# Kernel tuning notes

Hardware: AMD Instinct MI355X
Metric: run time of the kernel (lower is better)

The kernel has to match this reference:

```python
import jax, jax.numpy as jnp
import numpy as np

B, CIN, COUT, H, W, K, G = 2, 256, 256, 128, 128, 3, 4
PAD = (K - 1) // 2


def setup_inputs() -> dict:
    key = jax.random.key(0)
    k1, k2, k3, k4 = jax.random.split(key, 4)
    x = jax.random.normal(k1, (B, CIN, H, W), dtype=jnp.float32)
    # conv_offset: 1x1 conv, out channels = G*2*K*K. (Zero-init in the module; use
    # small random weights so offsets are non-trivial for correctness testing.)
    w_offset = jax.random.normal(k2, (G * 2 * K * K, CIN), dtype=jnp.float32) * 0.01
    b_offset = jax.random.normal(k3, (G * 2 * K * K,), dtype=jnp.float32) * 0.5
    # DeformConv weight (bias=False in mmcv DeformConv)
    w_deform = jax.random.normal(k4, (COUT, CIN, K, K), dtype=jnp.float32) * (1.0 / np.sqrt(CIN * K * K))
    return {"x": x, "w_offset": w_offset, "b_offset": b_offset, "w_deform": w_deform}


def _bilinear_gather(img, y, x):
    """img: [B,G,Cg,H,W]; y,x: [B,G,H,W] float sample coords -> [B,G,Cg,H,W].
    Zero padding outside the image (mmcv DCN bilinear semantics)."""
    b, g, cg, h, w = img.shape
    imgf = img.reshape(b, g, cg, h * w)
    y0 = jnp.floor(y)
    x0 = jnp.floor(x)
    out = jnp.zeros((b, g, cg, h * w), img.dtype)
    for yy, xx in ((y0, x0), (y0, x0 + 1.0), (y0 + 1.0, x0), (y0 + 1.0, x0 + 1.0)):
        wgt = (1.0 - jnp.abs(y - yy)) * (1.0 - jnp.abs(x - xx))
        valid = (yy >= 0) & (yy < h) & (xx >= 0) & (xx < w)
        wgt = jnp.where(valid, wgt, 0.0)
        yi = jnp.clip(yy, 0, h - 1).astype(jnp.int32)
        xi = jnp.clip(xx, 0, w - 1).astype(jnp.int32)
        idx = (yi * w + xi).reshape(b, g, 1, h * w)
        vals = jnp.take_along_axis(imgf, jnp.broadcast_to(idx, (b, g, cg, h * w)), axis=3)
        out = out + wgt.reshape(b, g, 1, h * w) * vals
    return out.reshape(b, g, cg, h, w)


def reference(x, w_offset, b_offset, w_deform):
    b, cin, h, w = x.shape
    cout, _, k, _ = w_deform.shape
    pad = (k - 1) // 2
    # 1x1 offset conv
    offset = jnp.einsum('bchw,oc->bohw', x, w_offset) + b_offset[None, :, None, None]
    g = offset.shape[1] // (2 * k * k)
    off = offset.reshape(b, g, k * k, 2, h, w)  # (dy, dx) per kernel tap, mmcv layout
    xg = x.reshape(b, g, cin // g, h, w)
    hh = jnp.arange(h, dtype=x.dtype)[:, None]
    ww = jnp.arange(w, dtype=x.dtype)[None, :]
    out = jnp.zeros((b, cout, h, w), x.dtype)
    for i in range(k):
        for j in range(k):
            t = i * k + j
            ys = hh - pad + i + off[:, :, t, 0]  # [B,G,H,W]
            xs = ww - pad + j + off[:, :, t, 1]
            samp = _bilinear_gather(xg, ys, xs).reshape(b, cin, h, w)
            out = out + jnp.einsum('bchw,oc->bohw', samp, w_deform[:, :, i, j])
    return jax.nn.relu(out)
```

## Files before the change

kernel.cpp:

```cpp
#include <hip/hip_runtime.h>
#include <stdint.h>

#define HW    16384
#define CIN   256
#define COUT  256
#define Hh    128
#define Ww    128
#define OFFC  72

typedef __attribute__((ext_vector_type(4))) float    f32x4;
typedef __attribute__((ext_vector_type(2))) _Float16 f16x2;
typedef __attribute__((ext_vector_type(8))) _Float16 f16x8;
typedef unsigned short u16;
typedef unsigned int   u32;

__device__ __forceinline__ u16 f2h(float f) { return __builtin_bit_cast(u16, (_Float16)f); }
__device__ __forceinline__ u32 pk2(float f) { u32 h = f2h(f); return h | (h << 16); }
__device__ __forceinline__ f16x2 bch(u32 u) { return __builtin_bit_cast(f16x2, u); }

__global__ __launch_bounds__(256) void kprep(const float* __restrict__ x, const float* __restrict__ wd,
                                             const float* __restrict__ wo, u16* __restrict__ xt,
                                             u16* __restrict__ wfrag, u16* __restrict__ wfrag2) {
  __shared__ float smem[9216];
  int blk = blockIdx.x;
  if (blk < 2048) {
    int bg = blk >> 8;
    int p0 = (blk & 255) << 6;
    const float* src = x + (size_t)bg * 64 * HW + p0;
    #pragma unroll
    for (int r = 0; r < 16; ++r) {
      int idx = threadIdx.x + 256 * r;
      int c = idx >> 6, px = idx & 63;
      smem[c * 65 + px] = src[(size_t)c * HW + px];
    }
    __syncthreads();
    int px = threadIdx.x >> 2, seg = threadIdx.x & 3;
    u32 w[8];
    #pragma unroll
    for (int k = 0; k < 8; ++k) {
      float lo = smem[(seg * 16 + 2 * k) * 65 + px];
      float hi = smem[(seg * 16 + 2 * k + 1) * 65 + px];
      w[k] = (u32)f2h(lo) | ((u32)f2h(hi) << 16);
    }
    u16* dst = xt + ((size_t)bg * HW + p0 + px) * 64 + seg * 16;
    *(uint4*)dst       = make_uint4(w[0], w[1], w[2], w[3]);
    *(uint4*)(dst + 8) = make_uint4(w[4], w[5], w[6], w[7]);
  } else if (blk < 2112) {
    int bb = blk - 2048;
    int nt = bb & 15;
    int g  = bb >> 4;
    const float* src = wd + (size_t)(nt * 16) * 2304 + (size_t)g * 64 * 9;
    #pragma unroll
    for (int r = 0; r < 36; ++r) {
      int idx = threadIdx.x + 256 * r;
      int cl  = idx / 576;
      int rem = idx - cl * 576;
      smem[cl * 576 + rem] = src[(size_t)cl * 2304 + rem];
    }
    __syncthreads();
    #pragma unroll
    for (int r = 0; r < 36; ++r) {
      int o    = threadIdx.x + 256 * r;
      int j    = o & 7;
      int lane = (o >> 3) & 63;
      int kcl  = o >> 9;
      int t = kcl >> 1, half = kcl & 1;
      int n = lane & 15, q = lane >> 4;
      int cg = half * 32 + q * 8 + j;
      float v = smem[n * 576 + cg * 9 + t];
      int kc = (g * 9 + t) * 2 + half;
      wfrag[(size_t)((kc * 16 + nt) * 64 + lane) * 8 + j] = f2h(v);
    }
  } else {
    int e = (blk - 2112) * 256 + threadIdx.x;
    int j = e & 7;
    int lane = (e >> 3) & 63;
    int idx = e >> 9;
    int kc = idx / 5, nt = idx - 5 * kc;
    int n16 = lane & 15, q = lane >> 4;
    int oc = nt * 16 + n16;
    int c  = kc * 32 + q * 8 + j;
    float v = (oc < OFFC) ? wo[(size_t)oc * CIN + c] : 0.f;
    wfrag2[e] = f2h(v);
  }
}

__global__ __launch_bounds__(256) void k1(const u16* __restrict__ xt, const u16* __restrict__ wfrag2,
                                          const float* __restrict__ bo, float* __restrict__ off) {
  int gw = (blockIdx.x << 2) + (threadIdx.x >> 6);
  int lane = threadIdx.x & 63, n16 = lane & 15, q = lane >> 4;
  int b  = gw >> 10;
  int p0 = (gw & 1023) << 4;
  f32x4 acc[5];
  #pragma unroll
  for (int nt = 0; nt < 5; ++nt) {
    int oc = nt * 16 + n16;
    float bv = (oc < OFFC) ? bo[oc] : 0.f;
    acc[nt] = (f32x4){bv, bv, bv, bv};
  }
  const u16* xtb = xt + (size_t)b * 4 * HW * 64;
  #pragma unroll
  for (int kc = 0; kc < 8; ++kc) {
    int g = kc >> 1;
    f16x8 af = __builtin_bit_cast(f16x8,
        *(const uint4*)(xtb + ((size_t)g * HW + p0 + n16) * 64 + (kc & 1) * 32 + q * 8));
    #pragma unroll
    for (int nt = 0; nt < 5; ++nt) {
      f16x8 bf = __builtin_bit_cast(f16x8, *(const uint4*)(wfrag2 + (size_t)(((kc * 5 + nt) << 6) + lane) * 8));
      acc[nt] = __builtin_amdgcn_mfma_f32_16x16x32_f16(af, bf, acc[nt], 0, 0, 0);
    }
  }
  float* ob = off + (size_t)b * OFFC * HW;
  #pragma unroll
  for (int nt = 0; nt < 5; ++nt) {
    int oc = nt * 16 + n16;
    if (oc < OFFC)
      *(f32x4*)(ob + (size_t)oc * HW + p0 + q * 4) = acc[nt];
  }
}

__device__ __forceinline__ void mkpre(float yy, float xx, int* ob, u32* wp) {
  float y0f = floorf(yy), x0f = floorf(xx);
  float fy = yy - y0f, fx = xx - x0f;
  int y0 = (int)y0f, x0 = (int)x0f;
  int y1 = y0 + 1, x1 = x0 + 1;
  float vy0 = (y0 >= 0 && y0 < Hh) ? 1.f : 0.f;
  float vy1 = (y1 >= 0 && y1 < Hh) ? 1.f : 0.f;
  float vx0 = (x0 >= 0 && x0 < Ww) ? 1.f : 0.f;
  float vx1 = (x1 >= 0 && x1 < Ww) ? 1.f : 0.f;
  wp[0] = pk2((1.f - fy) * (1.f - fx) * vy0 * vx0);
  wp[1] = pk2((1.f - fy) * fx * vy0 * vx1);
  wp[2] = pk2(fy * (1.f - fx) * vy1 * vx0);
  wp[3] = pk2(fy * fx * vy1 * vx1);
  int cy0 = min(max(y0, 0), Hh - 1), cy1 = min(max(y1, 0), Hh - 1);
  int cx0 = min(max(x0, 0), Ww - 1), cx1 = min(max(x1, 0), Ww - 1);
  ob[0] = (cy0 * Ww + cx0) << 7;
  ob[1] = (cy0 * Ww + cx1) << 7;
  ob[2] = (cy1 * Ww + cx0) << 7;
  ob[3] = (cy1 * Ww + cx1) << 7;
}

__device__ __forceinline__ uint4 bil16(uint4 a, uint4 b, uint4 c, uint4 d, const u32* wp) {
  f16x2 W0 = bch(wp[0]), W1 = bch(wp[1]), W2 = bch(wp[2]), W3 = bch(wp[3]);
  uint4 r;
  { f16x2 s = bch(a.x) * W0 + bch(b.x) * W1 + bch(c.x) * W2 + bch(d.x) * W3; r.x = __builtin_bit_cast(u32, s); }
  { f16x2 s = bch(a.y) * W0 + bch(b.y) * W1 + bch(c.y) * W2 + bch(d.y) * W3; r.y = __builtin_bit_cast(u32, s); }
  { f16x2 s = bch(a.z) * W0 + bch(b.z) * W1 + bch(c.z) * W2 + bch(d.z) * W3; r.z = __builtin_bit_cast(u32, s); }
  { f16x2 s = bch(a.w) * W0 + bch(b.w) * W1 + bch(c.w) * W2 + bch(d.w) * W3; r.w = __builtin_bit_cast(u32, s); }
  return r;
}

__global__ __launch_bounds__(256, 2) void k2(const u16* __restrict__ xt, const float* __restrict__ off,
                                             const u16* __restrict__ wfrag, float* __restrict__ out) {
  __shared__ u16 astage[8192];
  int tid = threadIdx.x;
  int lane = tid & 63, n16 = lane & 15, q = tid >> 4 & 3;
  int wv = tid >> 6;
  int b  = blockIdx.x >> 8;
  int p0 = (blockIdx.x & 255) << 6;
  int h  = p0 >> 7, w0 = p0 & 127;
  int pxg = p0 + wv * 16 + n16;
  float fh = (float)h;
  float fx = (float)(w0 + wv * 16 + n16);
  const float* offp = off + (size_t)b * OFFC * HW;
  const char*  xtb  = (const char*)xt + (size_t)b * 4 * HW * 128;
  int chb = q * 16;

  f32x4 acc[4][4];
  #pragma unroll
  for (int mt = 0; mt < 4; ++mt)
    #pragma unroll
    for (int j = 0; j < 4; ++j) acc[mt][j] = (f32x4){0.f, 0.f, 0.f, 0.f};

  float dy1, dx1;
  {
    float dy0 = offp[pxg];
    float dx0 = offp[(size_t)HW + pxg];
    dy1 = offp[(size_t)2 * HW + pxg];
    dx1 = offp[(size_t)3 * HW + pxg];
    int ob[4]; u32 wp[4];
    mkpre(fh - 1.f + dy0, fx - 1.f + dx0, ob, wp);
    uint4 c0[4], c1[4];
    #pragma unroll
    for (int c = 0; c < 4; ++c) {
      c0[c] = *(const uint4*)(xtb + ob[c] + chb);
      c1[c] = *(const uint4*)(xtb + ob[c] + chb + 64);
    }
    *(uint4*)&astage[(wv * 2 + 0) * 512 + lane * 8] = bil16(c0[0], c0[1], c0[2], c0[3], wp);
    *(uint4*)&astage[(wv * 2 + 1) * 512 + lane * 8] = bil16(c1[0], c1[1], c1[2], c1[3], wp);
  }
  __syncthreads();

  #pragma unroll 1
  for (int gt = 0; gt < 36; ++gt) {
    int buf = gt & 1;
    uint4 d0[4], d1[4];
    u32 wp[4];
    if (gt < 35) {
      int gtn = gt + 1;
      int g1 = (gtn * 57) >> 9;
      int t  = gtn - g1 * 9;
      int i  = (t * 683) >> 11;
      int j  = t - i * 3;
      int ob[4];
      mkpre(fh + (float)(i - 1) + dy1, fx + (float)(j - 1) + dx1, ob, wp);
      const char* xg = xtb + (size_t)g1 * HW * 128;
      #pragma unroll
      for (int c = 0; c < 4; ++c) {
        d0[c] = *(const uint4*)(xg + ob[c] + chb);
        d1[c] = *(const uint4*)(xg + ob[c] + chb + 64);
      }
      if (gt < 34) {
        dy1 = offp[(size_t)(2 * gt + 4) * HW + pxg];
        dx1 = offp[(size_t)(2 * gt + 5) * HW + pxg];
      }
    }
    const u16* wb = wfrag + ((size_t)((gt * 2) * 16 + wv * 4) * 64 + lane) * 8;
    f16x8 af[4][2];
    uint4 bf[2][4];
    #pragma unroll
    for (int hh = 0; hh < 2; ++hh) {
      #pragma unroll
      for (int j = 0; j < 4; ++j)
        bf[hh][j] = *(const uint4*)(wb + (size_t)(hh * 16 + j) * 512);
      #pragma unroll
      for (int mt = 0; mt < 4; ++mt)
        af[mt][hh] = __builtin_bit_cast(f16x8,
            *(const uint4*)&astage[(buf * 8 + mt * 2 + hh) * 512 + lane * 8]);
    }
    #pragma unroll
    for (int hh = 0; hh < 2; ++hh)
      #pragma unroll
      for (int mt = 0; mt < 4; ++mt)
        #pragma unroll
        for (int j = 0; j < 4; ++j)
          acc[mt][j] = __builtin_amdgcn_mfma_f32_16x16x32_f16(
              af[mt][hh], __builtin_bit_cast(f16x8, bf[hh][j]), acc[mt][j], 0, 0, 0);
    if (gt < 35) {
      int ib = (buf ^ 1) * 8 + wv * 2;
      *(uint4*)&astage[(ib + 0) * 512 + lane * 8] = bil16(d0[0], d0[1], d0[2], d0[3], wp);
      *(uint4*)&astage[(ib + 1) * 512 + lane * 8] = bil16(d1[0], d1[1], d1[2], d1[3], wp);
      __syncthreads();
    }
  }

  float* op = out + (size_t)b * COUT * HW + p0;
  #pragma unroll
  for (int mt = 0; mt < 4; ++mt)
    #pragma unroll
    for (int j = 0; j < 4; ++j) {
      f32x4 v = acc[mt][j];
      #pragma unroll
      for (int r = 0; r < 4; ++r) v[r] = fmaxf(v[r], 0.f);
      int cout = wv * 64 + j * 16 + n16;
      *(f32x4*)(op + (size_t)cout * HW + mt * 16 + q * 4) = v;
    }
}

extern "C" void kernel_launch(void* const* d_in, const int* in_sizes, int n_in,
                              void* d_out, int out_size, void* d_ws, size_t ws_size,
                              hipStream_t stream) {
  const float* x  = (const float*)d_in[0];
  const float* wo = (const float*)d_in[1];
  const float* bo = (const float*)d_in[2];
  const float* wd = (const float*)d_in[3];
  float* out = (float*)d_out;

  u16*   xtp    = (u16*)d_ws;
  u16*   wfrag  = (u16*)((char*)d_ws + 16777216);
  u16*   wfrag2 = (u16*)((char*)d_ws + 16777216 + 1179648);
  float* off    = (float*)((char*)d_ws + 16777216 + 1179648 + 40960);

  kprep<<<2192, 256, 0, stream>>>(x, wd, wo, xtp, wfrag, wfrag2);
  k1   <<<512,  256, 0, stream>>>(xtp, wfrag2, bo, off);
  k2   <<<512,  256, 0, stream>>>(xtp, off, wfrag, out);
}
```

Before: 198.4 us.

## Fuse offset conv into deform kernel and triple-buffer the gather pipeline

Removes the separate offset-conv kernel. Each k2 block now computes its own 72 offset channels for its 64 pixels with MFMA and keeps them in shared memory, which drops a launch and the global write and read of the offset tensor. The main loop changes from a double-buffered stage to a three-slot ring, with B-fragment loads issued one step ahead so gathers overlap MFMA work. The cost is more shared memory and more registers (two gather sets and two B-fragment sets), which may lower occupancy or cause spills.

```diff
diff --git a/kernel.cpp b/kernel.cpp
--- a/kernel.cpp
+++ b/kernel.cpp
@@ -82,40 +82,6 @@
     int c  = kc * 32 + q * 8 + j;
     float v = (oc < OFFC) ? wo[(size_t)oc * CIN + c] : 0.f;
     wfrag2[e] = f2h(v);
-  }
-}
-
-__global__ __launch_bounds__(256) void k1(const u16* __restrict__ xt, const u16* __restrict__ wfrag2,
-                                          const float* __restrict__ bo, float* __restrict__ off) {
-  int gw = (blockIdx.x << 2) + (threadIdx.x >> 6);
-  int lane = threadIdx.x & 63, n16 = lane & 15, q = lane >> 4;
-  int b  = gw >> 10;
-  int p0 = (gw & 1023) << 4;
-  f32x4 acc[5];
-  #pragma unroll
-  for (int nt = 0; nt < 5; ++nt) {
-    int oc = nt * 16 + n16;
-    float bv = (oc < OFFC) ? bo[oc] : 0.f;
-    acc[nt] = (f32x4){bv, bv, bv, bv};
-  }
-  const u16* xtb = xt + (size_t)b * 4 * HW * 64;
-  #pragma unroll
-  for (int kc = 0; kc < 8; ++kc) {
-    int g = kc >> 1;
-    f16x8 af = __builtin_bit_cast(f16x8,
-        *(const uint4*)(xtb + ((size_t)g * HW + p0 + n16) * 64 + (kc & 1) * 32 + q * 8));
-    #pragma unroll
-    for (int nt = 0; nt < 5; ++nt) {
-      f16x8 bf = __builtin_bit_cast(f16x8, *(const uint4*)(wfrag2 + (size_t)(((kc * 5 + nt) << 6) + lane) * 8));
-      acc[nt] = __builtin_amdgcn_mfma_f32_16x16x32_f16(af, bf, acc[nt], 0, 0, 0);
-    }
-  }
-  float* ob = off + (size_t)b * OFFC * HW;
-  #pragma unroll
-  for (int nt = 0; nt < 5; ++nt) {
-    int oc = nt * 16 + n16;
-    if (oc < OFFC)
-      *(f32x4*)(ob + (size_t)oc * HW + p0 + q * 4) = acc[nt];
   }
 }
 
@@ -150,21 +116,55 @@
   return r;
 }
 
-__global__ __launch_bounds__(256, 2) void k2(const u16* __restrict__ xt, const float* __restrict__ off,
-                                             const u16* __restrict__ wfrag, float* __restrict__ out) {
-  __shared__ u16 astage[8192];
+__global__ __launch_bounds__(256, 2) void k2(const u16* __restrict__ xt, const u16* __restrict__ wfrag2,
+                                             const float* __restrict__ bo, const u16* __restrict__ wfrag,
+                                             float* __restrict__ out) {
+  __shared__ u16   astage[3 * 4096];
+  __shared__ float offl[36 * 128];
   int tid = threadIdx.x;
-  int lane = tid & 63, n16 = lane & 15, q = tid >> 4 & 3;
+  int lane = tid & 63, n16 = lane & 15, q = (tid >> 4) & 3;
   int wv = tid >> 6;
   int b  = blockIdx.x >> 8;
   int p0 = (blockIdx.x & 255) << 6;
   int h  = p0 >> 7, w0 = p0 & 127;
-  int pxg = p0 + wv * 16 + n16;
+  const char* xtb = (const char*)xt + (size_t)b * 4 * HW * 128;
+
+  {
+    f32x4 oacc[5];
+    #pragma unroll
+    for (int nt = 0; nt < 5; ++nt) {
+      int oc = nt * 16 + n16;
+      float bv = (oc < OFFC) ? bo[oc] : 0.f;
+      oacc[nt] = (f32x4){bv, bv, bv, bv};
+    }
+    #pragma unroll
+    for (int kc = 0; kc < 8; ++kc) {
+      int g = kc >> 1;
+      f16x8 af = __builtin_bit_cast(f16x8, *(const uint4*)(xtb +
+          ((size_t)(g * HW + p0 + wv * 16 + n16)) * 128 + (kc & 1) * 64 + q * 16));
+      #pragma unroll
+      for (int nt = 0; nt < 5; ++nt) {
+        f16x8 bf = __builtin_bit_cast(f16x8, *(const uint4*)(wfrag2 + (size_t)(((kc * 5 + nt) << 6) + lane) * 8));
+        oacc[nt] = __builtin_amdgcn_mfma_f32_16x16x32_f16(af, bf, oacc[nt], 0, 0, 0);
+      }
+    }
+    #pragma unroll
+    for (int nt = 0; nt < 5; ++nt) {
+      int oc = nt * 16 + n16;
+      if (oc < OFFC) {
+        int gt = oc >> 1, comp = oc & 1;
+        #pragma unroll
+        for (int r = 0; r < 4; ++r)
+          offl[(gt * 64 + wv * 16 + q * 4 + r) * 2 + comp] = oacc[nt][r];
+      }
+    }
+  }
+  __syncthreads();
+
   float fh = (float)h;
   float fx = (float)(w0 + wv * 16 + n16);
-  const float* offp = off + (size_t)b * OFFC * HW;
-  const char*  xtb  = (const char*)xt + (size_t)b * 4 * HW * 128;
   int chb = q * 16;
+  int pxl = wv * 16 + n16;
 
   f32x4 acc[4][4];
   #pragma unroll
@@ -172,76 +172,73 @@
     #pragma unroll
     for (int j = 0; j < 4; ++j) acc[mt][j] = (f32x4){0.f, 0.f, 0.f, 0.f};
 
-  float dy1, dx1;
-  {
-    float dy0 = offp[pxg];
-    float dx0 = offp[(size_t)HW + pxg];
-    dy1 = offp[(size_t)2 * HW + pxg];
-    dx1 = offp[(size_t)3 * HW + pxg];
-    int ob[4]; u32 wp[4];
-    mkpre(fh - 1.f + dy0, fx - 1.f + dx0, ob, wp);
-    uint4 c0[4], c1[4];
+  auto issue = [&](int gt, uint4* d, u32* wp) {
+    float2 o = *(const float2*)&offl[(gt * 64 + pxl) * 2];
+    int g = (gt * 57) >> 9;
+    int t = gt - g * 9;
+    int i = (t * 683) >> 11;
+    int j = t - i * 3;
+    int ob[4];
+    mkpre(fh + (float)(i - 1) + o.x, fx + (float)(j - 1) + o.y, ob, wp);
+    const char* xg = xtb + (size_t)g * HW * 128;
     #pragma unroll
     for (int c = 0; c < 4; ++c) {
-      c0[c] = *(const uint4*)(xtb + ob[c] + chb);
-      c1[c] = *(const uint4*)(xtb + ob[c] + chb + 64);
-    }
-    *(uint4*)&astage[(wv * 2 + 0) * 512 + lane * 8] = bil16(c0[0], c0[1], c0[2], c0[3], wp);
-    *(uint4*)&astage[(wv * 2 + 1) * 512 + lane * 8] = bil16(c1[0], c1[1], c1[2], c1[3], wp);
-  }
-  __syncthreads();
-
-  #pragma unroll 1
-  for (int gt = 0; gt < 36; ++gt) {
-    int buf = gt & 1;
-    uint4 d0[4], d1[4];
-    u32 wp[4];
-    if (gt < 35) {
-      int gtn = gt + 1;
-      int g1 = (gtn * 57) >> 9;
-      int t  = gtn - g1 * 9;
-      int i  = (t * 683) >> 11;
-      int j  = t - i * 3;
-      int ob[4];
-      mkpre(fh + (float)(i - 1) + dy1, fx + (float)(j - 1) + dx1, ob, wp);
-      const char* xg = xtb + (size_t)g1 * HW * 128;
-      #pragma unroll
-      for (int c = 0; c < 4; ++c) {
-        d0[c] = *(const uint4*)(xg + ob[c] + chb);
-        d1[c] = *(const uint4*)(xg + ob[c] + chb + 64);
-      }
-      if (gt < 34) {
-        dy1 = offp[(size_t)(2 * gt + 4) * HW + pxg];
-        dx1 = offp[(size_t)(2 * gt + 5) * HW + pxg];
-      }
-    }
-    const u16* wb = wfrag + ((size_t)((gt * 2) * 16 + wv * 4) * 64 + lane) * 8;
-    f16x8 af[4][2];
-    uint4 bf[2][4];
+      d[c]     = *(const uint4*)(xg + ob[c] + chb);
+      d[4 + c] = *(const uint4*)(xg + ob[c] + chb + 64);
+    }
+  };
+  auto produce = [&](int slot, const uint4* d, const u32* wp) {
+    *(uint4*)&astage[(slot * 8 + wv * 2 + 0) * 512 + lane * 8] = bil16(d[0], d[1], d[2], d[3], wp);
+    *(uint4*)&astage[(slot * 8 + wv * 2 + 1) * 512 + lane * 8] = bil16(d[4], d[5], d[6], d[7], wp);
+  };
+  auto loadB = [&](int gt, uint4* bf) {
+    const u16* wb = wfrag + (size_t)gt * 16384 + (size_t)(wv * 4) * 512 + (size_t)lane * 8;
+    #pragma unroll
+    for (int hh = 0; hh < 2; ++hh)
+      #pragma unroll
+      for (int j = 0; j < 4; ++j)
+        bf[hh * 4 + j] = *(const uint4*)(wb + (size_t)(hh * 16 + j) * 512);
+  };
+  auto consume = [&](int slot, const uint4* bf) {
     #pragma unroll
     for (int hh = 0; hh < 2; ++hh) {
-      #pragma unroll
-      for (int j = 0; j < 4; ++j)
-        bf[hh][j] = *(const uint4*)(wb + (size_t)(hh * 16 + j) * 512);
+      f16x8 af[4];
       #pragma unroll
       for (int mt = 0; mt < 4; ++mt)
-        af[mt][hh] = __builtin_bit_cast(f16x8,
-            *(const uint4*)&astage[(buf * 8 + mt * 2 + hh) * 512 + lane * 8]);
-    }
-    #pragma unroll
-    for (int hh = 0; hh < 2; ++hh)
+        af[mt] = __builtin_bit_cast(f16x8,
+            *(const uint4*)&astage[(slot * 8 + mt * 2 + hh) * 512 + lane * 8]);
       #pragma unroll
       for (int mt = 0; mt < 4; ++mt)
         #pragma unroll
         for (int j = 0; j < 4; ++j)
           acc[mt][j] = __builtin_amdgcn_mfma_f32_16x16x32_f16(
-              af[mt][hh], __builtin_bit_cast(f16x8, bf[hh][j]), acc[mt][j], 0, 0, 0);
-    if (gt < 35) {
-      int ib = (buf ^ 1) * 8 + wv * 2;
-      *(uint4*)&astage[(ib + 0) * 512 + lane * 8] = bil16(d0[0], d0[1], d0[2], d0[3], wp);
-      *(uint4*)&astage[(ib + 1) * 512 + lane * 8] = bil16(d1[0], d1[1], d1[2], d1[3], wp);
+              af[mt], __builtin_bit_cast(f16x8, bf[hh * 4 + j]), acc[mt][j], 0, 0, 0);
+    }
+  };
+
+  uint4 dA[8], dB[8];
+  u32   wpA[4], wpB[4];
+  uint4 bfA[8], bfB[8];
+  issue(0, dA, wpA);
+  issue(1, dB, wpB);
+  produce(0, dA, wpA);
+  loadB(0, bfA);
+  __syncthreads();
+
+  #pragma unroll 1
+  for (int gt = 0; gt < 36; gt += 2) {
+    produce((gt + 1) % 3, dB, wpB);
+    if (gt + 2 < 36) issue(gt + 2, dA, wpA);
+    loadB(gt + 1, bfB);
+    __syncthreads();
+    consume(gt % 3, bfA);
+    if (gt + 2 < 36) {
+      produce((gt + 2) % 3, dA, wpA);
+      if (gt + 3 < 36) issue(gt + 3, dB, wpB);
+      loadB(gt + 2, bfA);
       __syncthreads();
     }
+    consume((gt + 1) % 3, bfB);
   }
 
   float* op = out + (size_t)b * COUT * HW + p0;
@@ -266,12 +263,10 @@
   const float* wd = (const float*)d_in[3];
   float* out = (float*)d_out;
 
-  u16*   xtp    = (u16*)d_ws;
-  u16*   wfrag  = (u16*)((char*)d_ws + 16777216);
-  u16*   wfrag2 = (u16*)((char*)d_ws + 16777216 + 1179648);
-  float* off    = (float*)((char*)d_ws + 16777216 + 1179648 + 40960);
+  u16* xtp    = (u16*)d_ws;
+  u16* wfrag  = (u16*)((char*)d_ws + 16777216);
+  u16* wfrag2 = (u16*)((char*)d_ws + 16777216 + 1179648);
 
   kprep<<<2192, 256, 0, stream>>>(x, wd, wo, xtp, wfrag, wfrag2);
-  k1   <<<512,  256, 0, stream>>>(xtp, wfrag2, bo, off);
-  k2   <<<512,  256, 0, stream>>>(xtp, off, wfrag, out);
-}
+  k2   <<<512,  256, 0, stream>>>(xtp, wfrag2, bo, wfrag, out);
+}
```

New measurement: 198.3 us. Within noise of the previous version (-0.1%).
